# Kernel optimization log

Hardware: AMD Instinct MI355X
Metric: run time of the kernel (lower is better)

The kernel has to match this reference:

```python
import jax, jax.numpy as jnp
import numpy as np

B, C, A, H, W = 8, 64, 32, 64, 64  # batch, input_nf, atten_nf, height, width

def setup_inputs() -> dict:
    key = jax.random.key(0)
    k = jax.random.split(key, 5)
    scale = 1.0 / np.sqrt(C)
    return {
        "x":  jax.random.normal(k[0], (B, C, H, W), dtype=jnp.float32),
        "Wg": jax.random.uniform(k[1], (A, C), jnp.float32, -scale, scale),  # 1x1 conv kernel
        "bg": jax.random.uniform(k[2], (A,),   jnp.float32, -scale, scale),
        "Wh": jax.random.uniform(k[3], (A, C), jnp.float32, -scale, scale),
        "bh": jax.random.uniform(k[4], (A,),   jnp.float32, -scale, scale),
    }

def reference(x, Wg, bg, Wh, bh):
    b, c, h, w = x.shape
    n = h * w
    xf = x.reshape(b, c, n)                               # [B, C, N]
    g = jnp.einsum('ac,bcn->ban', Wg, xf) + bg[None, :, None]  # 1x1 conv == GEMM
    hq = jnp.einsum('ac,bcn->ban', Wh, xf) + bh[None, :, None]
    scores = jnp.einsum('ban,bam->bnm', g, hq)            # [B, N, N]
    alpha = jax.nn.softmax(scores, axis=2)
    r = jnp.einsum('bnm,bcm->bcn', alpha, xf)             # alpha @ x^T, back to [B,C,N]
    r = r.reshape(b, c, h, w)
    r = r + x  # is_residual=True
    return (jax.nn.relu(r), alpha)
```

## Files before the change

### kernel.cpp

```cpp
#include <hip/hip_runtime.h>
#include <hip/hip_bf16.h>
#include <math.h>

#define NB 8
#define NC 64
#define NA 32
#define NN 4096
#define NWAVE 8

typedef __attribute__((ext_vector_type(8))) short bf16x8;
typedef __attribute__((ext_vector_type(4))) short bf16x4;
typedef __attribute__((ext_vector_type(4))) float f32x4;

#if __has_builtin(__builtin_amdgcn_mfma_f32_16x16x16bf16_1k)
  #define HAVE_MFMA16 1
  #define MFMA16(A,B,C) __builtin_amdgcn_mfma_f32_16x16x16bf16_1k(A,B,C,0,0,0)
#elif __has_builtin(__builtin_amdgcn_mfma_f32_16x16x16_bf16)
  #define HAVE_MFMA16 1
  #define MFMA16(A,B,C) __builtin_amdgcn_mfma_f32_16x16x16_bf16(A,B,C,0,0,0)
#else
  #define HAVE_MFMA16 0
#endif

__device__ inline ushort f2bf(float f) {
  union { float f; unsigned u; } v; v.f = f;
  unsigned r = v.u + 0x7fffu + ((v.u >> 16) & 1u);
  return (ushort)(r >> 16);
}

__device__ inline bf16x8 pack8(const f32x4 a, const f32x4 b) {
  union { ushort us[8]; bf16x8 v; } u;
#pragma unroll
  for (int i = 0; i < 4; ++i) { u.us[i] = f2bf(a[i]); u.us[4 + i] = f2bf(b[i]); }
  return u.v;
}

__device__ inline uint2 packbf(const f32x4 p) {
  uint2 q;
  q.x = (uint)f2bf(p[0]) | ((uint)f2bf(p[1]) << 16);
  q.y = (uint)f2bf(p[2]) | ((uint)f2bf(p[3]) << 16);
  return q;
}

#if HAVE_MFMA16
__device__ inline bf16x4 pk4(const f32x4 p) {
  union { uint u[2]; bf16x4 v; } t;
  asm("v_cvt_pk_bf16_f32 %0, %1, %2" : "=v"(t.u[0]) : "v"(p[0]), "v"(p[1]));
  asm("v_cvt_pk_bf16_f32 %0, %1, %2" : "=v"(t.u[1]) : "v"(p[2]), "v"(p[3]));
  return t.v;
}
#endif

__global__ __launch_bounds__(256) void prep_kernel(
    const float* __restrict__ x, const float* __restrict__ Wg, const float* __restrict__ bg,
    const float* __restrict__ Wh, const float* __restrict__ bh,
    ushort* __restrict__ gT, ushort* __restrict__ hqT, ushort* __restrict__ xfb2)
{
  __shared__ float wg_s[NA * NC];
  __shared__ float wh_s[NA * NC];
  const int t = threadIdx.x;
  for (int i = t; i < NA * NC; i += 256) { wg_s[i] = Wg[i]; wh_s[i] = Wh[i]; }
  __syncthreads();

  const int gid = blockIdx.x * 256 + t;
  const int b = gid >> 12;
  const int n = gid & (NN - 1);
  const float* xb = x + (size_t)b * NC * NN + n;
  const size_t x2base = (size_t)b * NC * NN + (size_t)(n >> 4) * (NC * 16) + (n & 15);

  float accg[NA], acch[NA];
#pragma unroll
  for (int a = 0; a < NA; ++a) { accg[a] = 0.f; acch[a] = 0.f; }

  for (int c4 = 0; c4 < NC / 4; ++c4) {
    const float xv0 = xb[(size_t)(c4 * 4 + 0) * NN];
    const float xv1 = xb[(size_t)(c4 * 4 + 1) * NN];
    const float xv2 = xb[(size_t)(c4 * 4 + 2) * NN];
    const float xv3 = xb[(size_t)(c4 * 4 + 3) * NN];
    xfb2[x2base + (size_t)(c4 * 4 + 0) * 16] = f2bf(xv0);
    xfb2[x2base + (size_t)(c4 * 4 + 1) * 16] = f2bf(xv1);
    xfb2[x2base + (size_t)(c4 * 4 + 2) * 16] = f2bf(xv2);
    xfb2[x2base + (size_t)(c4 * 4 + 3) * 16] = f2bf(xv3);
#pragma unroll
    for (int a = 0; a < NA; ++a) {
      const float4 wg4 = *(const float4*)&wg_s[a * NC + c4 * 4];
      const float4 wh4 = *(const float4*)&wh_s[a * NC + c4 * 4];
      accg[a] += wg4.x * xv0 + wg4.y * xv1 + wg4.z * xv2 + wg4.w * xv3;
      acch[a] += wh4.x * xv0 + wh4.y * xv1 + wh4.z * xv2 + wh4.w * xv3;
    }
  }

  const float LOG2E = 1.44269504088896340736f;
  ushort og[NA], oh[NA];
#pragma unroll
  for (int a = 0; a < NA; ++a) {
    og[a] = f2bf((accg[a] + bg[a]) * LOG2E);
    oh[a] = f2bf(acch[a] + bh[a]);
  }
  const size_t o = ((size_t)b * NN + n) * NA;
#pragma unroll
  for (int k = 0; k < 4; ++k) {
    uint4 vg, vh;
    vg.x = (uint)og[k*8+0] | ((uint)og[k*8+1] << 16);
    vg.y = (uint)og[k*8+2] | ((uint)og[k*8+3] << 16);
    vg.z = (uint)og[k*8+4] | ((uint)og[k*8+5] << 16);
    vg.w = (uint)og[k*8+6] | ((uint)og[k*8+7] << 16);
    vh.x = (uint)oh[k*8+0] | ((uint)oh[k*8+1] << 16);
    vh.y = (uint)oh[k*8+2] | ((uint)oh[k*8+3] << 16);
    vh.z = (uint)oh[k*8+4] | ((uint)oh[k*8+5] << 16);
    vh.w = (uint)oh[k*8+6] | ((uint)oh[k*8+7] << 16);
    *(uint4*)(gT  + o + k * 8) = vg;
    *(uint4*)(hqT + o + k * 8) = vh;
  }
}

__global__ __launch_bounds__(512, 4) void attn_kernel(
    const ushort* __restrict__ gT, const ushort* __restrict__ hqT,
    const ushort* __restrict__ xfb2, const float* __restrict__ x,
    float* __restrict__ outp, float* __restrict__ alpha)
{
  __shared__ float plds[NWAVE][32][32];
  __shared__ float rtile[32][65];
  __shared__ float Lp[NWAVE][32];
  __shared__ float LinvS[32];
#if !HAVE_MFMA16
  ushort (*pbuf)[32][36] = reinterpret_cast<ushort (*)[32][36]>(&plds[0][0][0]);
#endif

  const int tid = threadIdx.x;
  const int l  = tid & 63;
  const int w  = tid >> 6;
  const int lm = l & 15;
  const int lh = l >> 4;

  const int wgid = (blockIdx.x & 7) * 128 + (blockIdx.x >> 3);
  const int b  = wgid >> 7;
  const int n0 = (wgid & 127) << 5;

  const ushort* gB  = gT   + (size_t)b * NN * NA;
  const ushort* hB  = hqT  + (size_t)b * NN * NA;
  const ushort* xB2 = xfb2 + (size_t)b * NC * NN;

  bf16x8 gb0 = *(const bf16x8*)(gB + (size_t)(n0 + lm) * NA + lh * 8);
  bf16x8 gb1 = *(const bf16x8*)(gB + (size_t)(n0 + 16 + lm) * NA + lh * 8);
  const int mbase = w << 9;
  bf16x8 ha0 = *(const bf16x8*)(hB + (size_t)(mbase + lm) * NA + lh * 8);
  bf16x8 ha1 = *(const bf16x8*)(hB + (size_t)(mbase + 16 + lm) * NA + lh * 8);

  float* rflat = &rtile[0][0];
  for (int i = tid; i < 32 * 65; i += 512) rflat[i] = 0.f;

  const f32x4 zz = {0.f, 0.f, 0.f, 0.f};
  f32x4 racc[2][4];
#pragma unroll
  for (int gi = 0; gi < 2; ++gi)
#pragma unroll
    for (int ci = 0; ci < 4; ++ci) racc[gi][ci] = zz;

  float sume0 = 0.f, sume1 = 0.f;
  for (int mc = 0; mc < 16; ++mc) {
    const int m0 = mbase + (mc << 5);
    const int m1 = mbase + (((mc + 1) & 15) << 5);
    const int t0 = m0 >> 4;
    const bf16x8 na0 = *(const bf16x8*)(hB + (size_t)(m1 + lm) * NA + lh * 8);
    const bf16x8 na1 = *(const bf16x8*)(hB + (size_t)(m1 + 16 + lm) * NA + lh * 8);
#if HAVE_MFMA16
    bf16x4 xv0[4], xv1[4];
#pragma unroll
    for (int ci = 0; ci < 4; ++ci) {
      xv0[ci] = *(const bf16x4*)(xB2 + (size_t)t0       * (NC * 16) + (ci * 16 + lm) * 16 + lh * 4);
      xv1[ci] = *(const bf16x4*)(xB2 + (size_t)(t0 + 1) * (NC * 16) + (ci * 16 + lm) * 16 + lh * 4);
    }
#else
    bf16x8 xv[4];
#pragma unroll
    for (int ci = 0; ci < 4; ++ci)
      xv[ci] = *(const bf16x8*)(xB2 + (size_t)(t0 + (lh >> 1)) * (NC * 16) + (ci * 16 + lm) * 16 + (lh & 1) * 8);
#endif

    const f32x4 s00 = __builtin_amdgcn_mfma_f32_16x16x32_bf16(ha0, gb0, zz, 0, 0, 0);
    const f32x4 s10 = __builtin_amdgcn_mfma_f32_16x16x32_bf16(ha1, gb0, zz, 0, 0, 0);
    const f32x4 s01 = __builtin_amdgcn_mfma_f32_16x16x32_bf16(ha0, gb1, zz, 0, 0, 0);
    const f32x4 s11 = __builtin_amdgcn_mfma_f32_16x16x32_bf16(ha1, gb1, zz, 0, 0, 0);

    f32x4 e00, e10, e01, e11;
#pragma unroll
    for (int r = 0; r < 4; ++r) {
      e00[r] = exp2f(s00[r]);
      e10[r] = exp2f(s10[r]);
      e01[r] = exp2f(s01[r]);
      e11[r] = exp2f(s11[r]);
      sume0 += e00[r] + e10[r];
      sume1 += e01[r] + e11[r];
    }

#if HAVE_MFMA16
    const bf16x4 A00 = pk4(e00);
    const bf16x4 A01 = pk4(e10);
    const bf16x4 A10 = pk4(e01);
    const bf16x4 A11 = pk4(e11);
#pragma unroll
    for (int ci = 0; ci < 4; ++ci) {
      racc[0][ci] = MFMA16(A00, xv0[ci], racc[0][ci]);
      racc[0][ci] = MFMA16(A01, xv1[ci], racc[0][ci]);
      racc[1][ci] = MFMA16(A10, xv0[ci], racc[1][ci]);
      racc[1][ci] = MFMA16(A11, xv1[ci], racc[1][ci]);
    }
#else
    *(uint2*)&pbuf[w][lm][lh * 4]           = packbf(e00);
    *(uint2*)&pbuf[w][lm][16 + lh * 4]      = packbf(e10);
    *(uint2*)&pbuf[w][16 + lm][lh * 4]      = packbf(e01);
    *(uint2*)&pbuf[w][16 + lm][16 + lh * 4] = packbf(e11);
    union UB { uint4 u; bf16x8 v; } ua, ub;
    {
      const uint2 a0 = *(const uint2*)&pbuf[w][lm][lh * 8];
      const uint2 a1 = *(const uint2*)&pbuf[w][lm][lh * 8 + 4];
      ua.u = make_uint4(a0.x, a0.y, a1.x, a1.y);
      const uint2 b0 = *(const uint2*)&pbuf[w][16 + lm][lh * 8];
      const uint2 b1 = *(const uint2*)&pbuf[w][16 + lm][lh * 8 + 4];
      ub.u = make_uint4(b0.x, b0.y, b1.x, b1.y);
    }
#pragma unroll
    for (int ci = 0; ci < 4; ++ci) {
      racc[0][ci] = __builtin_amdgcn_mfma_f32_16x16x32_bf16(ua.v, xv[ci], racc[0][ci], 0, 0, 0);
      racc[1][ci] = __builtin_amdgcn_mfma_f32_16x16x32_bf16(ub.v, xv[ci], racc[1][ci], 0, 0, 0);
    }
#endif
    ha0 = na0; ha1 = na1;
  }

  sume0 += __shfl_xor(sume0, 16); sume0 += __shfl_xor(sume0, 32);
  sume1 += __shfl_xor(sume1, 16); sume1 += __shfl_xor(sume1, 32);
  if (l < 16) { Lp[w][l] = sume0; Lp[w][16 + l] = sume1; }
  __syncthreads();

  float Ls0 = 0.f, Ls1 = 0.f;
#pragma unroll
  for (int ww = 0; ww < NWAVE; ++ww) { Ls0 += Lp[ww][lm]; Ls1 += Lp[ww][16 + lm]; }
  const float blog0 = -log2f(Ls0);
  const float blog1 = -log2f(Ls1);

  if (tid < 32) {
    float s = 0.f;
#pragma unroll
    for (int ww = 0; ww < NWAVE; ++ww) s += Lp[ww][tid];
    LinvS[tid] = 1.0f / s;
  }

#pragma unroll
  for (int gi = 0; gi < 2; ++gi)
#pragma unroll
    for (int ci = 0; ci < 4; ++ci)
#pragma unroll
      for (int r = 0; r < 4; ++r)
        atomicAdd(&rtile[gi * 16 + lh * 4 + r][ci * 16 + lm], racc[gi][ci][r]);
  __syncthreads();

  {
    const int c  = tid >> 3;
    const int j4 = (tid & 7) << 2;
    f32x4 v;
#pragma unroll
    for (int k = 0; k < 4; ++k) v[k] = rtile[j4 + k][c] * LinvS[j4 + k];
    const size_t oo = ((size_t)b * NC + c) * NN + n0 + j4;
    const f32x4 xr = *(const f32x4*)(x + oo);
#pragma unroll
    for (int k = 0; k < 4; ++k) {
      const float t = v[k] + xr[k];
      v[k] = t > 0.f ? t : 0.f;
    }
    __builtin_nontemporal_store(v, (f32x4*)(outp + oo));
  }

  const f32x4 bias0 = {blog0, blog0, blog0, blog0};
  const f32x4 bias1 = {blog1, blog1, blog1, blog1};
  float* aB = alpha + ((size_t)b * NN + n0) * NN;
  const int k7   = lm & 7;
  const int nrow = l >> 3;
  const int uu   = l & 7;

  for (int mc = 0; mc < 16; ++mc) {
    const int m0 = mbase + (mc << 5);
    const int m1 = mbase + (((mc + 1) & 15) << 5);
    const bf16x8 na0 = *(const bf16x8*)(hB + (size_t)(m1 + lm) * NA + lh * 8);
    const bf16x8 na1 = *(const bf16x8*)(hB + (size_t)(m1 + 16 + lm) * NA + lh * 8);

    const f32x4 s00 = __builtin_amdgcn_mfma_f32_16x16x32_bf16(ha0, gb0, bias0, 0, 0, 0);
    const f32x4 s10 = __builtin_amdgcn_mfma_f32_16x16x32_bf16(ha1, gb0, bias0, 0, 0, 0);
    const f32x4 s01 = __builtin_amdgcn_mfma_f32_16x16x32_bf16(ha0, gb1, bias1, 0, 0, 0);
    const f32x4 s11 = __builtin_amdgcn_mfma_f32_16x16x32_bf16(ha1, gb1, bias1, 0, 0, 0);

    f32x4 p00, p10, p01, p11;
#pragma unroll
    for (int r = 0; r < 4; ++r) {
      p00[r] = exp2f(s00[r]);
      p10[r] = exp2f(s10[r]);
      p01[r] = exp2f(s01[r]);
      p11[r] = exp2f(s11[r]);
    }

    *(f32x4*)&plds[w][lm]     [((lh    ) ^ k7) << 2] = p00;
    *(f32x4*)&plds[w][lm]     [((lh + 4) ^ k7) << 2] = p10;
    *(f32x4*)&plds[w][16 + lm][((lh    ) ^ k7) << 2] = p01;
    *(f32x4*)&plds[w][16 + lm][((lh + 4) ^ k7) << 2] = p11;

#pragma unroll
    for (int j = 0; j < 4; ++j) {
      const int row = j * 8 + nrow;
      const f32x4 pv = *(const f32x4*)&plds[w][row][(uu ^ (row & 7)) << 2];
      *(f32x4*)(aB + (size_t)row * NN + m0 + uu * 4) = pv;
    }
    ha0 = na0; ha1 = na1;
  }
}

extern "C" void kernel_launch(void* const* d_in, const int* in_sizes, int n_in,
                              void* d_out, int out_size, void* d_ws, size_t ws_size,
                              hipStream_t stream) {
  const float* x  = (const float*)d_in[0];
  const float* Wg = (const float*)d_in[1];
  const float* bg = (const float*)d_in[2];
  const float* Wh = (const float*)d_in[3];
  const float* bh = (const float*)d_in[4];

  float* outp  = (float*)d_out;
  float* alpha = outp + (size_t)NB * NC * NN;

  ushort* gT   = (ushort*)d_ws;
  ushort* hqT  = gT + (size_t)NB * NN * NA;
  ushort* xfb2 = hqT + (size_t)NB * NN * NA;

  prep_kernel<<<NB * NN / 256, 256, 0, stream>>>(x, Wg, bg, Wh, bh, gT, hqT, xfb2);
  attn_kernel<<<NB * (NN / 32), 512, 0, stream>>>(gT, hqT, xfb2, x, outp, alpha);
}
```

Baseline: 229.7 us.

## Stage alpha rows in a shared block-wide window for full-row nontemporal stores

The alpha write-out phase no longer stages each wave's 32x32 probability tile in a private LDS buffer. All waves now fill a shared 32x512 window (padded stride), with each wave covering an interleaved column slice. Every two chunks the block synchronizes, and each wave writes four full 512-wide row segments to global memory with nontemporal stores, giving long contiguous bursts instead of short 128-byte pieces. The cost is extra block-wide barriers, a larger LDS footprint that may lower occupancy, and a changed column-to-wave assignment.

```diff
diff --git a/kernel.cpp b/kernel.cpp
--- a/kernel.cpp
+++ b/kernel.cpp
@@ -7,6 +7,7 @@
 #define NA 32
 #define NN 4096
 #define NWAVE 8
+#define WSTRIDE 524
 
 typedef __attribute__((ext_vector_type(8))) short bf16x8;
 typedef __attribute__((ext_vector_type(4))) short bf16x4;
@@ -119,12 +120,12 @@
     const ushort* __restrict__ xfb2, const float* __restrict__ x,
     float* __restrict__ outp, float* __restrict__ alpha)
 {
-  __shared__ float plds[NWAVE][32][32];
+  __shared__ float winbuf[32][WSTRIDE];
   __shared__ float rtile[32][65];
   __shared__ float Lp[NWAVE][32];
   __shared__ float LinvS[32];
 #if !HAVE_MFMA16
-  ushort (*pbuf)[32][36] = reinterpret_cast<ushort (*)[32][36]>(&plds[0][0][0]);
+  ushort (*pbuf)[32][36] = reinterpret_cast<ushort (*)[32][36]>(&winbuf[0][0]);
 #endif
 
   const int tid = threadIdx.x;
@@ -271,17 +272,20 @@
     }
     __builtin_nontemporal_store(v, (f32x4*)(outp + oo));
   }
+  __syncthreads();
 
   const f32x4 bias0 = {blog0, blog0, blog0, blog0};
   const f32x4 bias1 = {blog1, blog1, blog1, blog1};
   float* aB = alpha + ((size_t)b * NN + n0) * NN;
-  const int k7   = lm & 7;
-  const int nrow = l >> 3;
-  const int uu   = l & 7;
+  const int wb = w << 5;
+
+  ha0 = *(const bf16x8*)(hB + (size_t)(wb + lm) * NA + lh * 8);
+  ha1 = *(const bf16x8*)(hB + (size_t)(wb + 16 + lm) * NA + lh * 8);
 
   for (int mc = 0; mc < 16; ++mc) {
-    const int m0 = mbase + (mc << 5);
-    const int m1 = mbase + (((mc + 1) & 15) << 5);
+    const int cs = ((mc & 1) << 8) + wb;
+    const int mn = (mc + 1) & 15;
+    const int m1 = ((mn >> 1) << 9) + ((mn & 1) << 8) + wb;
     const bf16x8 na0 = *(const bf16x8*)(hB + (size_t)(m1 + lm) * NA + lh * 8);
     const bf16x8 na1 = *(const bf16x8*)(hB + (size_t)(m1 + 16 + lm) * NA + lh * 8);
 
@@ -299,16 +303,25 @@
       p11[r] = exp2f(s11[r]);
     }
 
-    *(f32x4*)&plds[w][lm]     [((lh    ) ^ k7) << 2] = p00;
-    *(f32x4*)&plds[w][lm]     [((lh + 4) ^ k7) << 2] = p10;
-    *(f32x4*)&plds[w][16 + lm][((lh    ) ^ k7) << 2] = p01;
-    *(f32x4*)&plds[w][16 + lm][((lh + 4) ^ k7) << 2] = p11;
-
-#pragma unroll
-    for (int j = 0; j < 4; ++j) {
-      const int row = j * 8 + nrow;
-      const f32x4 pv = *(const f32x4*)&plds[w][row][(uu ^ (row & 7)) << 2];
-      *(f32x4*)(aB + (size_t)row * NN + m0 + uu * 4) = pv;
+    *(f32x4*)&winbuf[lm]     [cs + lh * 4]      = p00;
+    *(f32x4*)&winbuf[lm]     [cs + 16 + lh * 4] = p10;
+    *(f32x4*)&winbuf[16 + lm][cs + lh * 4]      = p01;
+    *(f32x4*)&winbuf[16 + lm][cs + 16 + lh * 4] = p11;
+
+    if (mc & 1) {
+      asm volatile("s_waitcnt lgkmcnt(0)\n\ts_barrier" ::: "memory");
+
+      const size_t mw = (size_t)(mc >> 1) << 9;
+#pragma unroll
+      for (int j = 0; j < 4; ++j) {
+        const int row = (w << 2) + j;
+        const f32x4 v0 = *(const f32x4*)&winbuf[row][l * 4];
+        const f32x4 v1 = *(const f32x4*)&winbuf[row][256 + l * 4];
+        float* rp = aB + (size_t)row * NN + mw;
+        __builtin_nontemporal_store(v0, (f32x4*)(rp + l * 4));
+        __builtin_nontemporal_store(v1, (f32x4*)(rp + 256 + l * 4));
+      }
+      asm volatile("s_waitcnt lgkmcnt(0)\n\ts_barrier" ::: "memory");
     }
     ha0 = na0; ha1 = na1;
   }
```

Result: no change. 233.3 us (+1.6%).
